# Kernel optimization log

Measured on AMD Instinct MI355X. Metric: run time of the kernel, lower is better.

## Reference

```python
import jax, jax.numpy as jnp
import numpy as np
import math

L, D, H, DH, DFF, V, NB, MAXD = 4, 512, 8, 64, 1024, 32128, 32, 128
B, S = 2, 2048
EPS = 1e-6


def gelu_new(x):
    return 0.5 * x * (1.0 + jnp.tanh(math.sqrt(2.0 / math.pi) * (x + 0.044715 * x ** 3)))


def t5_layernorm(x, w):
    var = jnp.mean(jnp.square(x.astype(jnp.float32)), axis=-1, keepdims=True)
    return w * (x * jax.lax.rsqrt(var + EPS))


def relative_position_bucket(rel_pos, num_buckets=NB, max_distance=MAXD):
    # bidirectional T5 bucketing
    nb = num_buckets // 2
    buckets = (rel_pos > 0).astype(jnp.int32) * nb
    rp = jnp.abs(rel_pos)
    max_exact = nb // 2
    is_small = rp < max_exact
    rp_large = max_exact + (
        jnp.log(jnp.maximum(rp, 1).astype(jnp.float32) / max_exact)
        / math.log(max_distance / max_exact) * (nb - max_exact)
    ).astype(jnp.int32)
    rp_large = jnp.minimum(rp_large, nb - 1)
    return buckets + jnp.where(is_small, rp, rp_large)


def compute_bias(rel_bias_table, q_len, k_len):
    ctx = jnp.arange(q_len)[:, None]
    mem = jnp.arange(k_len)[None, :]
    buckets = relative_position_bucket(mem - ctx)              # [S, S]
    vals = rel_bias_table[buckets]                             # [S, S, H]
    return jnp.transpose(vals, (2, 0, 1))[None]                # [1, H, S, S]


def setup_inputs() -> dict:
    key = jax.random.key(0)
    ks = jax.random.split(key, 12)
    s = 0.02
    return {
        "input_ids": jax.random.randint(ks[0], (B, S), 0, V),
        "embed": jax.random.normal(ks[1], (V, D), jnp.float32) * s,
        "Wq": jax.random.normal(ks[2], (L, D, H * DH), jnp.float32) * s,
        "Wk": jax.random.normal(ks[3], (L, D, H * DH), jnp.float32) * s,
        "Wv": jax.random.normal(ks[4], (L, D, H * DH), jnp.float32) * s,
        "Wo": jax.random.normal(ks[5], (L, H * DH, D), jnp.float32) * s,
        "rel_bias": jax.random.normal(ks[6], (NB, H), jnp.float32) * s,
        "wi0": jax.random.normal(ks[7], (L, D, DFF), jnp.float32) * s,
        "wi1": jax.random.normal(ks[8], (L, D, DFF), jnp.float32) * s,
        "wo_ffn": jax.random.normal(ks[9], (L, DFF, D), jnp.float32) * s,
        "ln0_w": jnp.ones((L, D), jnp.float32),
        "ln1_w": jnp.ones((L, D), jnp.float32),
        "final_ln_w": jnp.ones((D,), jnp.float32),
    }


def encoder_forward(input_ids, embed, Wq, Wk, Wv, Wo, rel_bias, wi0, wi1, wo_ffn, ln0_w, ln1_w, final_ln_w):
    x = embed[input_ids]                                       # [B, S, D]
    pos_bias = compute_bias(rel_bias, S, S)                    # [1, H, S, S], reused across layers
    for i in range(L):
        # --- self-attention (T5: no 1/sqrt(d) scaling) ---
        h = t5_layernorm(x, ln0_w[i])
        q = (h @ Wq[i]).reshape(B, S, H, DH)
        k = (h @ Wk[i]).reshape(B, S, H, DH)
        v = (h @ Wv[i]).reshape(B, S, H, DH)
        scores = jnp.einsum('bqhd,bkhd->bhqk', q, k) + pos_bias
        attn = jax.nn.softmax(scores, axis=-1)
        o = jnp.einsum('bhqk,bkhd->bqhd', attn, v).reshape(B, S, H * DH)
        x = x + o @ Wo[i]
        # --- gated-GELU FFN ---
        h = t5_layernorm(x, ln1_w[i])
        g = gelu_new(h @ wi0[i]) * (h @ wi1[i])
        x = x + g @ wo_ffn[i]
    out = t5_layernorm(x, final_ln_w)
    return out, pos_bias


def reference(input_ids, embed, Wq, Wk, Wv, Wo, rel_bias, wi0, wi1, wo_ffn, ln0_w, ln1_w, final_ln_w):
    return encoder_forward(input_ids, embed, Wq, Wk, Wv, Wo, rel_bias, wi0, wi1, wo_ffn, ln0_w, ln1_w, final_ln_w)
```

## Files before the change

### kernel.cpp

```cpp
#include <hip/hip_runtime.h>

#define NTOK 4096

typedef float f32x4 __attribute__((ext_vector_type(4)));
typedef short s16x8 __attribute__((ext_vector_type(8)));
typedef unsigned short u16x4 __attribute__((ext_vector_type(4)));
typedef unsigned short u16x8 __attribute__((ext_vector_type(8)));

__device__ __forceinline__ unsigned short fbf(float f) {
  unsigned int u = __float_as_uint(f);
  return (unsigned short)((u + 0x7FFFu + ((u >> 16) & 1u)) >> 16);
}
__device__ __forceinline__ float bf2f(unsigned short s) {
  return __uint_as_float(((unsigned int)s) << 16);
}
__device__ __forceinline__ float gelu_new_f(float x) {
  float inner = 0.7978845608028654f * (x + 0.044715f * x * x * x);
  return 0.5f * x * (1.0f + tanhf(inner));
}

__device__ __forceinline__ void gl_lds16(const void* g, void* l) {
  __builtin_amdgcn_global_load_lds(
      (const __attribute__((address_space(1))) unsigned int*)g,
      (__attribute__((address_space(3))) unsigned int*)l, 16, 0, 0);
}

__global__ void embed_kernel(const int* __restrict__ ids, const float* __restrict__ emb,
                             float* __restrict__ x) {
  int tok = blockIdx.x;
  int id = ids[tok];
  int t = threadIdx.x;
  *(float4*)(x + (size_t)tok * 512 + t * 4) = *(const float4*)(emb + (size_t)id * 512 + t * 4);
}

__global__ void build_dbias_kernel(const float* __restrict__ rel_bias, float* __restrict__ dbias) {
  int d = blockIdx.x * 256 + threadIdx.x;
  if (d >= 4096) return;
  int rel = d - 2047;
  int bucket = (rel > 0) ? 16 : 0;
  int rp = rel < 0 ? -rel : rel;
  if (rp < 8) {
    bucket += rp;
  } else {
    float v = logf((float)rp / 8.0f) / logf(16.0f) * 8.0f;
    int rl = 8 + (int)v;
    bucket += (rl < 15) ? rl : 15;
  }
  for (int hh = 0; hh < 8; ++hh)
    dbias[hh * 4096 + d] = rel_bias[bucket * 8 + hh];
}

__global__ void posbias_kernel(const float* __restrict__ dbias, float* __restrict__ out1) {
  size_t g = (size_t)blockIdx.x * 256 + threadIdx.x;
  int k4 = (int)(g & 511) * 4;
  int qq = (int)((g >> 9) & 2047);
  int hh = (int)(g >> 20);
  const float* src = dbias + hh * 4096 + (k4 - qq + 2047);
  *(float4*)(out1 + g * 4) = make_float4(src[0], src[1], src[2], src[3]);
}

__global__ void rmsnorm_bf16_kernel(const float* __restrict__ x, const float* __restrict__ w,
                                    unsigned short* __restrict__ out) {
  int tok = blockIdx.x;
  int t = threadIdx.x;
  float4 v = *(const float4*)(x + (size_t)tok * 512 + t * 4);
  float ss = v.x * v.x + v.y * v.y + v.z * v.z + v.w * v.w;
  for (int m = 1; m < 64; m <<= 1) ss += __shfl_xor(ss, m, 64);
  __shared__ float part[2];
  if ((t & 63) == 0) part[t >> 6] = ss;
  __syncthreads();
  float scale = rsqrtf((part[0] + part[1]) * (1.0f / 512.0f) + 1e-6f);
  float4 wv = *(const float4*)(w + t * 4);
  u16x4 o = {fbf(wv.x * v.x * scale), fbf(wv.y * v.y * scale),
             fbf(wv.z * v.z * scale), fbf(wv.w * v.w * scale)};
  *(u16x4*)(out + (size_t)tok * 512 + t * 4) = o;
}

__global__ void rmsnorm_f32_kernel(const float* __restrict__ x, const float* __restrict__ w,
                                   float* __restrict__ out) {
  int tok = blockIdx.x;
  int t = threadIdx.x;
  float4 v = *(const float4*)(x + (size_t)tok * 512 + t * 4);
  float ss = v.x * v.x + v.y * v.y + v.z * v.z + v.w * v.w;
  for (int m = 1; m < 64; m <<= 1) ss += __shfl_xor(ss, m, 64);
  __shared__ float part[2];
  if ((t & 63) == 0) part[t >> 6] = ss;
  __syncthreads();
  float scale = rsqrtf((part[0] + part[1]) * (1.0f / 512.0f) + 1e-6f);
  float4 wv = *(const float4*)(w + t * 4);
  *(float4*)(out + (size_t)tok * 512 + t * 4) =
      make_float4(wv.x * v.x * scale, wv.y * v.y * scale, wv.z * v.z * scale, wv.w * v.w * scale);
}

__global__ void transw_kernel(const float* S0, const float* S1, const float* S2, const float* S3,
                              unsigned short* D0, unsigned short* D1, unsigned short* D2,
                              unsigned short* D3, int R, int C) {
  __shared__ float tile[32][33];
  int mat = blockIdx.z >> 2, layer = blockIdx.z & 3;
  const float* src = (mat == 0 ? S0 : mat == 1 ? S1 : mat == 2 ? S2 : S3) + (size_t)layer * R * C;
  unsigned short* dst = (mat == 0 ? D0 : mat == 1 ? D1 : mat == 2 ? D2 : D3) + (size_t)layer * R * C;
  int t = threadIdx.x;
  int r0 = blockIdx.y * 32, c0 = blockIdx.x * 32;
  int tr = t >> 3, tc = (t & 7) * 4;
  float4 v = *(const float4*)(src + (size_t)(r0 + tr) * C + c0 + tc);
  tile[tr][tc] = v.x; tile[tr][tc + 1] = v.y; tile[tr][tc + 2] = v.z; tile[tr][tc + 3] = v.w;
  __syncthreads();
  u16x4 o = {fbf(tile[tc + 0][tr]), fbf(tile[tc + 1][tr]),
             fbf(tile[tc + 2][tr]), fbf(tile[tc + 3][tr])};
  *(u16x4*)(dst + (size_t)(c0 + tr) * R + r0 + tc) = o;
}

__global__ __launch_bounds__(256) void gemm64_kernel(
    const unsigned short* __restrict__ A,
    const unsigned short* B0, const unsigned short* B1, const unsigned short* B2,
    void* C0, void* C1, void* C2, const float* __restrict__ Res,
    int M, int N, int K, int m0, int m1, int m2) {
  __shared__ unsigned short As[2][64 * 64];
  __shared__ unsigned short Bs[2][64 * 64];
  const int z = blockIdx.z;
  const unsigned short* B = (z == 0) ? B0 : (z == 1) ? B1 : B2;
  void* Cptr = (z == 0) ? C0 : (z == 1) ? C1 : C2;
  const int mode = (z == 0) ? m0 : (z == 1) ? m1 : m2;
  const int t = threadIdx.x, lane = t & 63, w = t >> 6;
  const int quad = lane >> 4, c = lane & 15;
  const int wr = w >> 1, wc = w & 1;
  const int row0 = blockIdx.y * 64, col0 = blockIdx.x * 64;
  const int ar = t >> 3, aj = t & 7;
  const int asrc8 = (aj ^ (ar & 7)) * 8;
  const unsigned short* Agl = A + (size_t)(row0 + ar) * K + asrc8;
  const unsigned short* Bgl = B + (size_t)(col0 + ar) * K + asrc8;
  f32x4 acc[2][2];
#pragma unroll
  for (int i = 0; i < 2; ++i)
#pragma unroll
    for (int j = 0; j < 2; ++j) { f32x4 zz = {0.f, 0.f, 0.f, 0.f}; acc[i][j] = zz; }

  gl_lds16(Agl, &As[0][w * 512]);
  gl_lds16(Agl + 32 * (size_t)K, &As[0][2048 + w * 512]);
  gl_lds16(Bgl, &Bs[0][w * 512]);
  gl_lds16(Bgl + 32 * (size_t)K, &Bs[0][2048 + w * 512]);
  __syncthreads();

  int p = 0;
  for (int k0 = 0; k0 < K; k0 += 64) {
    if (k0 + 64 < K) {
      gl_lds16(Agl + k0 + 64, &As[p ^ 1][w * 512]);
      gl_lds16(Agl + k0 + 64 + 32 * (size_t)K, &As[p ^ 1][2048 + w * 512]);
      gl_lds16(Bgl + k0 + 64, &Bs[p ^ 1][w * 512]);
      gl_lds16(Bgl + k0 + 64 + 32 * (size_t)K, &Bs[p ^ 1][2048 + w * 512]);
    }
    s16x8 af[2][2], bf[2][2];
#pragma unroll
    for (int rb = 0; rb < 2; ++rb) {
      int r = wr * 32 + rb * 16 + c;
      int n = wc * 32 + rb * 16 + c;
#pragma unroll
      for (int ks = 0; ks < 2; ++ks) {
        af[rb][ks] = *(const s16x8*)&As[p][r * 64 + (((ks * 4 + quad) ^ (r & 7)) << 3)];
        bf[rb][ks] = *(const s16x8*)&Bs[p][n * 64 + (((ks * 4 + quad) ^ (n & 7)) << 3)];
      }
    }
#pragma unroll
    for (int rb = 0; rb < 2; ++rb)
#pragma unroll
      for (int cb = 0; cb < 2; ++cb)
#pragma unroll
        for (int ks = 0; ks < 2; ++ks)
          acc[rb][cb] = __builtin_amdgcn_mfma_f32_16x16x32_bf16(af[rb][ks], bf[cb][ks], acc[rb][cb], 0, 0, 0);
    __syncthreads();
    p ^= 1;
  }

  const int mb = row0 + wr * 32 + quad * 4;
  const int nb = col0 + wc * 32 + c;
  if (mode == 0) {
    unsigned short* Cp = (unsigned short*)Cptr;
#pragma unroll
    for (int rb = 0; rb < 2; ++rb)
#pragma unroll
      for (int cb = 0; cb < 2; ++cb) {
        size_t base = (size_t)(mb + rb * 16) * N + nb + cb * 16;
#pragma unroll
        for (int reg = 0; reg < 4; ++reg) Cp[base + (size_t)reg * N] = fbf(acc[rb][cb][reg]);
      }
  } else if (mode == 1) {
    unsigned short* Cp = (unsigned short*)Cptr;
#pragma unroll
    for (int rb = 0; rb < 2; ++rb)
#pragma unroll
      for (int cb = 0; cb < 2; ++cb) {
        u16x4 pk = {fbf(acc[rb][cb][0]), fbf(acc[rb][cb][1]), fbf(acc[rb][cb][2]), fbf(acc[rb][cb][3])};
        *(u16x4*)&Cp[(size_t)(nb + cb * 16) * M + mb + rb * 16] = pk;
      }
  } else {
    float* Cf = (float*)Cptr;
#pragma unroll
    for (int rb = 0; rb < 2; ++rb)
#pragma unroll
      for (int cb = 0; cb < 2; ++cb)
#pragma unroll
        for (int reg = 0; reg < 4; ++reg) {
          size_t o = (size_t)(mb + rb * 16 + reg) * N + nb + cb * 16;
          Cf[o] = Res[o] + acc[rb][cb][reg];
        }
  }
}

__global__ __launch_bounds__(256) void gemm64_wo_kernel(
    const unsigned short* __restrict__ O0, const unsigned short* __restrict__ O1,
    const float* __restrict__ lsum, const unsigned short* __restrict__ Bw,
    float* __restrict__ Cf, const float* __restrict__ Res) {
  __shared__ unsigned short As[2][64 * 64];
  __shared__ unsigned short Bs[2][64 * 64];
  const int K = 512, N = 512;
  const int t = threadIdx.x, lane = t & 63, w = t >> 6;
  const int quad = lane >> 4, c = lane & 15;
  const int wr = w >> 1, wc = w & 1;
  const int row0 = blockIdx.y * 64, col0 = blockIdx.x * 64;
  const int ar = t >> 3, aj = t & 7;
  const int gc8 = (aj ^ (ar & 7)) * 8;
  const unsigned short* Bgl = Bw + (size_t)(col0 + ar) * K + gc8;

  size_t abase[2];
#pragma unroll
  for (int v = 0; v < 2; ++v) {
    int tok = row0 + ar + 32 * v;
    abase[v] = (size_t)((tok >> 11) * 16384 + (tok & 2047));
  }

  u16x8 ap0[2], ap1[2];
  float asum[2];
  auto ldA = [&](int kt) {
#pragma unroll
    for (int v = 0; v < 2; ++v) {
      size_t gr = abase[v] + (size_t)kt * 2048;
      ap0[v] = *(const u16x8*)(O0 + gr * 64 + gc8);
      ap1[v] = *(const u16x8*)(O1 + gr * 64 + gc8);
      asum[v] = lsum[gr] + lsum[32768 + gr];
    }
  };
  auto wrA = [&](int pp) {
#pragma unroll
    for (int v = 0; v < 2; ++v) {
      float inv = 1.0f / asum[v];
      u16x8 o;
#pragma unroll
      for (int j = 0; j < 8; ++j)
        o[j] = fbf((bf2f(ap0[v][j]) + bf2f(ap1[v][j])) * inv);
      *(u16x8*)&As[pp][(ar + 32 * v) * 64 + aj * 8] = o;
    }
  };

  f32x4 acc[2][2];
#pragma unroll
  for (int i = 0; i < 2; ++i)
#pragma unroll
    for (int j = 0; j < 2; ++j) { f32x4 zz = {0.f, 0.f, 0.f, 0.f}; acc[i][j] = zz; }

  ldA(0);
  wrA(0);
  gl_lds16(Bgl, &Bs[0][w * 512]);
  gl_lds16(Bgl + 32 * (size_t)K, &Bs[0][2048 + w * 512]);
  __syncthreads();
  ldA(1);

  int p = 0;
  for (int i = 0; i < 8; ++i) {
    if (i < 7) {
      int k0n = (i + 1) * 64;
      gl_lds16(Bgl + k0n, &Bs[p ^ 1][w * 512]);
      gl_lds16(Bgl + k0n + 32 * (size_t)K, &Bs[p ^ 1][2048 + w * 512]);
      wrA(p ^ 1);
    }
    s16x8 af[2][2], bf[2][2];
#pragma unroll
    for (int rb = 0; rb < 2; ++rb) {
      int r = wr * 32 + rb * 16 + c;
      int n = wc * 32 + rb * 16 + c;
#pragma unroll
      for (int ks = 0; ks < 2; ++ks) {
        af[rb][ks] = *(const s16x8*)&As[p][r * 64 + (((ks * 4 + quad) ^ (r & 7)) << 3)];
        bf[rb][ks] = *(const s16x8*)&Bs[p][n * 64 + (((ks * 4 + quad) ^ (n & 7)) << 3)];
      }
    }
#pragma unroll
    for (int rb = 0; rb < 2; ++rb)
#pragma unroll
      for (int cb = 0; cb < 2; ++cb)
#pragma unroll
        for (int ks = 0; ks < 2; ++ks)
          acc[rb][cb] = __builtin_amdgcn_mfma_f32_16x16x32_bf16(af[rb][ks], bf[cb][ks], acc[rb][cb], 0, 0, 0);
    if (i < 6) ldA(i + 2);
    __syncthreads();
    p ^= 1;
  }

  const int mb = row0 + wr * 32 + quad * 4;
  const int nb = col0 + wc * 32 + c;
#pragma unroll
  for (int rb = 0; rb < 2; ++rb)
#pragma unroll
    for (int cb = 0; cb < 2; ++cb)
#pragma unroll
      for (int reg = 0; reg < 4; ++reg) {
        size_t o = (size_t)(mb + rb * 16 + reg) * N + nb + cb * 16;
        Cf[o] = Res[o] + acc[rb][cb][reg];
      }
}

__global__ __launch_bounds__(256) void gemm_ffn_kernel(
    const unsigned short* __restrict__ A, const unsigned short* __restrict__ B0g,
    const unsigned short* __restrict__ B1g, unsigned short* __restrict__ C) {
  __shared__ unsigned short As[2][128 * 64];
  __shared__ unsigned short Bs0[2][64 * 64];
  __shared__ unsigned short Bs1[2][64 * 64];
  const int t = threadIdx.x, lane = t & 63, w = t >> 6;
  const int quad = lane >> 4, c = lane & 15;
  const int wr = w >> 1, wc = w & 1;
  const int row0 = blockIdx.y * 128, col0 = blockIdx.x * 64;
  const int K = 512;
  f32x4 acc0[4][2], acc1[4][2];
#pragma unroll
  for (int i = 0; i < 4; ++i)
#pragma unroll
    for (int j = 0; j < 2; ++j) {
      f32x4 zz = {0.f, 0.f, 0.f, 0.f};
      acc0[i][j] = zz; acc1[i][j] = zz;
    }

  const int ar = t >> 3, aj = t & 7;
  const int asrc8 = (aj ^ (ar & 7)) * 8;
  const unsigned short* Agl = A + (size_t)(row0 + ar) * K + asrc8;
  const unsigned short* B0gl = B0g + (size_t)(col0 + ar) * K + asrc8;
  const unsigned short* B1gl = B1g + (size_t)(col0 + ar) * K + asrc8;

  auto stage = [&](int pp, int kk) {
    gl_lds16(Agl + kk, &As[pp][w * 512]);
    gl_lds16(Agl + kk + 32 * (size_t)K, &As[pp][2048 + w * 512]);
    gl_lds16(Agl + kk + 64 * (size_t)K, &As[pp][4096 + w * 512]);
    gl_lds16(Agl + kk + 96 * (size_t)K, &As[pp][6144 + w * 512]);
    gl_lds16(B0gl + kk, &Bs0[pp][w * 512]);
    gl_lds16(B0gl + kk + 32 * (size_t)K, &Bs0[pp][2048 + w * 512]);
    gl_lds16(B1gl + kk, &Bs1[pp][w * 512]);
    gl_lds16(B1gl + kk + 32 * (size_t)K, &Bs1[pp][2048 + w * 512]);
  };

  stage(0, 0);
  __syncthreads();

  int p = 0;
  for (int k0 = 0; k0 < K; k0 += 64) {
    if (k0 + 64 < K) stage(p ^ 1, k0 + 64);
    s16x8 af[4][2], bf0[2][2], bf1[2][2];
#pragma unroll
    for (int rb = 0; rb < 4; ++rb) {
      int r = wr * 64 + rb * 16 + c;
#pragma unroll
      for (int ks = 0; ks < 2; ++ks)
        af[rb][ks] = *(const s16x8*)&As[p][r * 64 + (((ks * 4 + quad) ^ (r & 7)) << 3)];
    }
#pragma unroll
    for (int cb = 0; cb < 2; ++cb) {
      int n = wc * 32 + cb * 16 + c;
#pragma unroll
      for (int ks = 0; ks < 2; ++ks) {
        bf0[cb][ks] = *(const s16x8*)&Bs0[p][n * 64 + (((ks * 4 + quad) ^ (n & 7)) << 3)];
        bf1[cb][ks] = *(const s16x8*)&Bs1[p][n * 64 + (((ks * 4 + quad) ^ (n & 7)) << 3)];
      }
    }
#pragma unroll
    for (int rb = 0; rb < 4; ++rb)
#pragma unroll
      for (int cb = 0; cb < 2; ++cb)
#pragma unroll
        for (int ks = 0; ks < 2; ++ks) {
          acc0[rb][cb] = __builtin_amdgcn_mfma_f32_16x16x32_bf16(af[rb][ks], bf0[cb][ks], acc0[rb][cb], 0, 0, 0);
          acc1[rb][cb] = __builtin_amdgcn_mfma_f32_16x16x32_bf16(af[rb][ks], bf1[cb][ks], acc1[rb][cb], 0, 0, 0);
        }
    __syncthreads();
    p ^= 1;
  }

  const int mb = row0 + wr * 64 + quad * 4;
  const int nb = col0 + wc * 32 + c;
#pragma unroll
  for (int rb = 0; rb < 4; ++rb)
#pragma unroll
    for (int cb = 0; cb < 2; ++cb) {
      size_t base = (size_t)(mb + rb * 16) * 1024 + nb + cb * 16;
#pragma unroll
      for (int reg = 0; reg < 4; ++reg)
        C[base + (size_t)reg * 1024] = fbf(gelu_new_f(acc0[rb][cb][reg]) * acc1[rb][cb][reg]);
    }
}

__global__ __launch_bounds__(256, 4) void attn_split_kernel(
    const unsigned short* __restrict__ qg, const unsigned short* __restrict__ kg,
    const unsigned short* __restrict__ vtg, const float* __restrict__ dbias,
    unsigned short* __restrict__ Op0, unsigned short* __restrict__ Op1,
    float* __restrict__ lsum) {
  __shared__ unsigned short Ks[64 * 64];
  __shared__ unsigned short Vs[64 * 64];
  __shared__ unsigned short Ps[4][16 * 64];
  __shared__ float Bb[128];
  const int b = blockIdx.z, hh = blockIdx.y;
  const int q0b = (blockIdx.x & 31) * 64;
  const int split = blockIdx.x >> 5;
  unsigned short* Op = (split == 0) ? Op0 : Op1;
  const int t = threadIdx.x, lane = t & 63, w = t >> 6;
  const int quad = lane >> 4, c = lane & 15;
  const int hd = hh * 64;
  s16x8 qf[2];
#pragma unroll
  for (int ks = 0; ks < 2; ++ks)
    qf[ks] = *(const s16x8*)(qg + (size_t)(b * 2048 + q0b + w * 16 + c) * 512 + hd + ks * 32 + quad * 8);
  f32x4 oacc[4];
  float psum[4];
#pragma unroll
  for (int i = 0; i < 4; ++i) {
    f32x4 zz = {0.f, 0.f, 0.f, 0.f};
    oacc[i] = zz; psum[i] = 0.f;
  }
  const int biasbase = hh * 4096 + 2047 - q0b - 63;
  const int rowloc = w * 16 + quad * 4;
  const int srow = t >> 3, sjj = t & 7;
  const unsigned short* kbase = kg + (size_t)(b * 2048) * 512 + hd;
  const unsigned short* vbase = vtg + (size_t)hd * 4096 + b * 2048;
  const int kt0 = split * 16;

  s16x8 kpre[2], vpre[2];
  float bpre;
  {
    int k0 = kt0 * 64;
#pragma unroll
    for (int v = 0; v < 2; ++v) {
      int row = srow + 32 * v;
      kpre[v] = *(const s16x8*)(kbase + (size_t)(k0 + row) * 512 + sjj * 8);
      vpre[v] = *(const s16x8*)(vbase + (size_t)row * 4096 + k0 + sjj * 8);
    }
    bpre = dbias[biasbase + k0 + (t & 127)];
  }

  for (int kt = kt0; kt < kt0 + 16; ++kt) {
    __syncthreads();
#pragma unroll
    for (int v = 0; v < 2; ++v) {
      int row = srow + 32 * v;
      int ch = (sjj ^ (row & 7)) << 3;
      *(s16x8*)&Ks[row * 64 + ch] = kpre[v];
      *(s16x8*)&Vs[row * 64 + ch] = vpre[v];
    }
    if (t < 128) Bb[t] = bpre;
    __syncthreads();
    {
      int k0n = (kt + 1 < kt0 + 16) ? (kt + 1) * 64 : kt * 64;
#pragma unroll
      for (int v = 0; v < 2; ++v) {
        int row = srow + 32 * v;
        kpre[v] = *(const s16x8*)(kbase + (size_t)(k0n + row) * 512 + sjj * 8);
        vpre[v] = *(const s16x8*)(vbase + (size_t)row * 4096 + k0n + sjj * 8);
      }
      bpre = dbias[biasbase + k0n + (t & 127)];
    }

    f32x4 s[4];
#pragma unroll
    for (int i = 0; i < 4; ++i) { f32x4 zz = {0.f, 0.f, 0.f, 0.f}; s[i] = zz; }
#pragma unroll
    for (int ks = 0; ks < 2; ++ks)
#pragma unroll
      for (int cb = 0; cb < 4; ++cb) {
        int n = cb * 16 + c;
        s16x8 kf = *(const s16x8*)&Ks[n * 64 + (((ks * 4 + quad) ^ (n & 7)) << 3)];
        s[cb] = __builtin_amdgcn_mfma_f32_16x16x32_bf16(qf[ks], kf, s[cb], 0, 0, 0);
      }
#pragma unroll
    for (int cb = 0; cb < 4; ++cb) {
      int col = cb * 16 + c;
      int chunkbase = (col >> 3);
#pragma unroll
      for (int reg = 0; reg < 4; ++reg) {
        float pp = __expf(s[cb][reg] + Bb[col - rowloc - reg + 63]);
        psum[reg] += pp;
        int rowp = quad * 4 + reg;
        Ps[w][rowp * 64 + ((chunkbase ^ (rowp & 7)) << 3) + (col & 7)] = fbf(pp);
      }
    }
#pragma unroll
    for (int ks = 0; ks < 2; ++ks) {
      s16x8 pf = *(const s16x8*)&Ps[w][c * 64 + (((ks * 4 + quad) ^ (c & 7)) << 3)];
#pragma unroll
      for (int cbo = 0; cbo < 4; ++cbo) {
        int n = cbo * 16 + c;
        s16x8 vf = *(const s16x8*)&Vs[n * 64 + (((ks * 4 + quad) ^ (n & 7)) << 3)];
        oacc[cbo] = __builtin_amdgcn_mfma_f32_16x16x32_bf16(pf, vf, oacc[cbo], 0, 0, 0);
      }
    }
  }
#pragma unroll
  for (int reg = 0; reg < 4; ++reg) {
    float ps = psum[reg];
    ps += __shfl_xor(ps, 1, 64);
    ps += __shfl_xor(ps, 2, 64);
    ps += __shfl_xor(ps, 4, 64);
    ps += __shfl_xor(ps, 8, 64);
    psum[reg] = ps;
  }
  const size_t obase = ((size_t)(b * 8 + hh) * 2048 + q0b + w * 16 + quad * 4);
#pragma unroll
  for (int cbo = 0; cbo < 4; ++cbo)
#pragma unroll
    for (int reg = 0; reg < 4; ++reg)
      Op[(obase + reg) * 64 + cbo * 16 + c] = fbf(oacc[cbo][reg]);
  if (c == 0) {
    const size_t lbase = (size_t)split * 32768 + (size_t)(b * 8 + hh) * 2048 + q0b + w * 16 + quad * 4;
#pragma unroll
    for (int reg = 0; reg < 4; ++reg) lsum[lbase + reg] = psum[reg];
  }
}

extern "C" void kernel_launch(void* const* d_in, const int* in_sizes, int n_in,
                              void* d_out, int out_size, void* d_ws, size_t ws_size,
                              hipStream_t stream) {
  const int*   ids      = (const int*)d_in[0];
  const float* embed    = (const float*)d_in[1];
  const float* Wq       = (const float*)d_in[2];
  const float* Wk       = (const float*)d_in[3];
  const float* Wv       = (const float*)d_in[4];
  const float* Wo       = (const float*)d_in[5];
  const float* rel_bias = (const float*)d_in[6];
  const float* wi0      = (const float*)d_in[7];
  const float* wi1      = (const float*)d_in[8];
  const float* wo_ffn   = (const float*)d_in[9];
  const float* ln0      = (const float*)d_in[10];
  const float* ln1      = (const float*)d_in[11];
  const float* final_ln = (const float*)d_in[12];
  float* out = (float*)d_out;
  char* wsb = (char*)d_ws;

  float*          x    = (float*)wsb;
  unsigned short* h    = (unsigned short*)(wsb + 8388608);
  unsigned short* qb   = (unsigned short*)(wsb + 12582912);
  unsigned short* kb   = (unsigned short*)(wsb + 16777216);
  unsigned short* vt   = (unsigned short*)(wsb + 20971520);
  unsigned short* wqT  = (unsigned short*)(wsb + 33554432);
  unsigned short* wkT  = (unsigned short*)(wsb + 35651584);
  unsigned short* wvT  = (unsigned short*)(wsb + 37748736);
  unsigned short* woT  = (unsigned short*)(wsb + 39845888);
  unsigned short* wi0T = (unsigned short*)(wsb + 41943040);
  unsigned short* wi1T = (unsigned short*)(wsb + 46137344);
  unsigned short* wofT = (unsigned short*)(wsb + 50331648);
  float*          dbias= (float*)(wsb + 54525952);
  unsigned short* t0b  = kb;
  unsigned short* Op0  = h;
  unsigned short* Op1  = (unsigned short*)(wsb + 25165824);
  float*          lsum = (float*)(wsb + 60817408);

  embed_kernel<<<NTOK, 128, 0, stream>>>(ids, embed, x);
  build_dbias_kernel<<<16, 256, 0, stream>>>(rel_bias, dbias);
  posbias_kernel<<<32768, 256, 0, stream>>>(dbias, out + 2097152);
  transw_kernel<<<dim3(16, 16, 16), 256, 0, stream>>>(Wq, Wk, Wv, Wo, wqT, wkT, wvT, woT, 512, 512);
  transw_kernel<<<dim3(32, 16, 8), 256, 0, stream>>>(wi0, wi1, wi0, wi0, wi0T, wi1T, wi0T, wi0T, 512, 1024);
  transw_kernel<<<dim3(16, 32, 4), 256, 0, stream>>>(wo_ffn, wo_ffn, wo_ffn, wo_ffn, wofT, wofT, wofT, wofT, 1024, 512);

  for (int l = 0; l < 4; ++l) {
    const unsigned short* wqT_l = wqT + (size_t)l * 262144;
    const unsigned short* wkT_l = wkT + (size_t)l * 262144;
    const unsigned short* wvT_l = wvT + (size_t)l * 262144;
    const unsigned short* woT_l = woT + (size_t)l * 262144;
    const unsigned short* wi0T_l = wi0T + (size_t)l * 524288;
    const unsigned short* wi1T_l = wi1T + (size_t)l * 524288;
    const unsigned short* wofT_l = wofT + (size_t)l * 524288;

    rmsnorm_bf16_kernel<<<NTOK, 128, 0, stream>>>(x, ln0 + l * 512, h);
    gemm64_kernel<<<dim3(8, 64, 3), 256, 0, stream>>>(h, wqT_l, wkT_l, wvT_l,
        qb, kb, vt, nullptr, NTOK, 512, 512, 0, 0, 1);
    attn_split_kernel<<<dim3(64, 8, 2), 256, 0, stream>>>(qb, kb, vt, dbias,
        Op0, Op1, lsum);
    gemm64_wo_kernel<<<dim3(8, 64), 256, 0, stream>>>(Op0, Op1, lsum, woT_l, x, x);
    rmsnorm_bf16_kernel<<<NTOK, 128, 0, stream>>>(x, ln1 + l * 512, h);
    gemm_ffn_kernel<<<dim3(16, 32), 256, 0, stream>>>(h, wi0T_l, wi1T_l, t0b);
    gemm64_kernel<<<dim3(8, 64, 1), 256, 0, stream>>>(t0b, wofT_l, wofT_l, wofT_l,
        x, x, x, x, NTOK, 512, 1024, 2, 2, 2);
  }
  rmsnorm_f32_kernel<<<NTOK, 128, 0, stream>>>(x, final_ln, out);
}
```

Baseline: 674.0 us.

## Fuse RMSNorm into GEMM prologues with sum-of-squares computed in residual epilogues

```diff
diff --git a/kernel.cpp b/kernel.cpp
--- a/kernel.cpp
+++ b/kernel.cpp
@@ -25,12 +25,23 @@
       (__attribute__((address_space(3))) unsigned int*)l, 16, 0, 0);
 }
 
+__global__ void zero_ssq_kernel(float* __restrict__ p) {
+  p[blockIdx.x * 256 + threadIdx.x] = 0.f;
+}
+
 __global__ void embed_kernel(const int* __restrict__ ids, const float* __restrict__ emb,
-                             float* __restrict__ x) {
+                             float* __restrict__ x, float* __restrict__ ssq0) {
   int tok = blockIdx.x;
   int id = ids[tok];
   int t = threadIdx.x;
-  *(float4*)(x + (size_t)tok * 512 + t * 4) = *(const float4*)(emb + (size_t)id * 512 + t * 4);
+  float4 v = *(const float4*)(emb + (size_t)id * 512 + t * 4);
+  *(float4*)(x + (size_t)tok * 512 + t * 4) = v;
+  float ss = v.x * v.x + v.y * v.y + v.z * v.z + v.w * v.w;
+  for (int m = 1; m < 64; m <<= 1) ss += __shfl_xor(ss, m, 64);
+  __shared__ float part[2];
+  if ((t & 63) == 0) part[t >> 6] = ss;
+  __syncthreads();
+  if (t == 0) ssq0[tok] = part[0] + part[1];
 }
 
 __global__ void build_dbias_kernel(const float* __restrict__ rel_bias, float* __restrict__ dbias) {
@@ -59,34 +70,12 @@
   *(float4*)(out1 + g * 4) = make_float4(src[0], src[1], src[2], src[3]);
 }
 
-__global__ void rmsnorm_bf16_kernel(const float* __restrict__ x, const float* __restrict__ w,
-                                    unsigned short* __restrict__ out) {
+__global__ void rmsnorm_f32_kernel(const float* __restrict__ x, const float* __restrict__ w,
+                                   const float* __restrict__ ssqv, float* __restrict__ out) {
   int tok = blockIdx.x;
   int t = threadIdx.x;
+  float scale = rsqrtf(ssqv[tok] * (1.0f / 512.0f) + 1e-6f);
   float4 v = *(const float4*)(x + (size_t)tok * 512 + t * 4);
-  float ss = v.x * v.x + v.y * v.y + v.z * v.z + v.w * v.w;
-  for (int m = 1; m < 64; m <<= 1) ss += __shfl_xor(ss, m, 64);
-  __shared__ float part[2];
-  if ((t & 63) == 0) part[t >> 6] = ss;
-  __syncthreads();
-  float scale = rsqrtf((part[0] + part[1]) * (1.0f / 512.0f) + 1e-6f);
-  float4 wv = *(const float4*)(w + t * 4);
-  u16x4 o = {fbf(wv.x * v.x * scale), fbf(wv.y * v.y * scale),
-             fbf(wv.z * v.z * scale), fbf(wv.w * v.w * scale)};
-  *(u16x4*)(out + (size_t)tok * 512 + t * 4) = o;
-}
-
-__global__ void rmsnorm_f32_kernel(const float* __restrict__ x, const float* __restrict__ w,
-                                   float* __restrict__ out) {
-  int tok = blockIdx.x;
-  int t = threadIdx.x;
-  float4 v = *(const float4*)(x + (size_t)tok * 512 + t * 4);
-  float ss = v.x * v.x + v.y * v.y + v.z * v.z + v.w * v.w;
-  for (int m = 1; m < 64; m <<= 1) ss += __shfl_xor(ss, m, 64);
-  __shared__ float part[2];
-  if ((t & 63) == 0) part[t >> 6] = ss;
-  __syncthreads();
-  float scale = rsqrtf((part[0] + part[1]) * (1.0f / 512.0f) + 1e-6f);
   float4 wv = *(const float4*)(w + t * 4);
   *(float4*)(out + (size_t)tok * 512 + t * 4) =
       make_float4(wv.x * v.x * scale, wv.y * v.y * scale, wv.z * v.z * scale, wv.w * v.w * scale);
@@ -110,44 +99,69 @@
   *(u16x4*)(dst + (size_t)(c0 + tr) * R + r0 + tc) = o;
 }
 
-__global__ __launch_bounds__(256) void gemm64_kernel(
-    const unsigned short* __restrict__ A,
+__global__ __launch_bounds__(256) void gemm64_qkv_kernel(
+    const float* __restrict__ X, const float* __restrict__ lnw, const float* __restrict__ ssqv,
     const unsigned short* B0, const unsigned short* B1, const unsigned short* B2,
-    void* C0, void* C1, void* C2, const float* __restrict__ Res,
-    int M, int N, int K, int m0, int m1, int m2) {
+    unsigned short* __restrict__ Cq, unsigned short* __restrict__ Ck,
+    unsigned short* __restrict__ Cv) {
   __shared__ unsigned short As[2][64 * 64];
   __shared__ unsigned short Bs[2][64 * 64];
+  const int K = 512, N = 512, M = NTOK;
   const int z = blockIdx.z;
   const unsigned short* B = (z == 0) ? B0 : (z == 1) ? B1 : B2;
-  void* Cptr = (z == 0) ? C0 : (z == 1) ? C1 : C2;
-  const int mode = (z == 0) ? m0 : (z == 1) ? m1 : m2;
   const int t = threadIdx.x, lane = t & 63, w = t >> 6;
   const int quad = lane >> 4, c = lane & 15;
   const int wr = w >> 1, wc = w & 1;
   const int row0 = blockIdx.y * 64, col0 = blockIdx.x * 64;
   const int ar = t >> 3, aj = t & 7;
-  const int asrc8 = (aj ^ (ar & 7)) * 8;
-  const unsigned short* Agl = A + (size_t)(row0 + ar) * K + asrc8;
-  const unsigned short* Bgl = B + (size_t)(col0 + ar) * K + asrc8;
+  const int chunk = aj ^ (ar & 7);
+  const unsigned short* Bgl = B + (size_t)(col0 + ar) * K + chunk * 8;
+
+  float scl[2];
+#pragma unroll
+  for (int v = 0; v < 2; ++v)
+    scl[v] = rsqrtf(ssqv[row0 + ar + 32 * v] * (1.0f / 512.0f) + 1e-6f);
+
+  float4 xv[2][2], wv_[2];
+  auto ldA = [&](int kt) {
+    const float* xp = X + (size_t)(row0 + ar) * 512 + kt * 64 + chunk * 8;
+    xv[0][0] = *(const float4*)xp; xv[0][1] = *(const float4*)(xp + 4);
+    xp += 32 * 512;
+    xv[1][0] = *(const float4*)xp; xv[1][1] = *(const float4*)(xp + 4);
+    const float* wp = lnw + kt * 64 + chunk * 8;
+    wv_[0] = *(const float4*)wp; wv_[1] = *(const float4*)(wp + 4);
+  };
+  auto wrA = [&](int pp) {
+#pragma unroll
+    for (int v = 0; v < 2; ++v) {
+      u16x8 o;
+      o[0] = fbf(xv[v][0].x * scl[v] * wv_[0].x); o[1] = fbf(xv[v][0].y * scl[v] * wv_[0].y);
+      o[2] = fbf(xv[v][0].z * scl[v] * wv_[0].z); o[3] = fbf(xv[v][0].w * scl[v] * wv_[0].w);
+      o[4] = fbf(xv[v][1].x * scl[v] * wv_[1].x); o[5] = fbf(xv[v][1].y * scl[v] * wv_[1].y);
+      o[6] = fbf(xv[v][1].z * scl[v] * wv_[1].z); o[7] = fbf(xv[v][1].w * scl[v] * wv_[1].w);
+      *(u16x8*)&As[pp][(ar + 32 * v) * 64 + aj * 8] = o;
+    }
+  };
+
   f32x4 acc[2][2];
 #pragma unroll
   for (int i = 0; i < 2; ++i)
 #pragma unroll
     for (int j = 0; j < 2; ++j) { f32x4 zz = {0.f, 0.f, 0.f, 0.f}; acc[i][j] = zz; }
 
-  gl_lds16(Agl, &As[0][w * 512]);
-  gl_lds16(Agl + 32 * (size_t)K, &As[0][2048 + w * 512]);
+  ldA(0);
+  wrA(0);
   gl_lds16(Bgl, &Bs[0][w * 512]);
   gl_lds16(Bgl + 32 * (size_t)K, &Bs[0][2048 + w * 512]);
   __syncthreads();
+  ldA(1);
 
   int p = 0;
-  for (int k0 = 0; k0 < K; k0 += 64) {
-    if (k0 + 64 < K) {
-      gl_lds16(Agl + k0 + 64, &As[p ^ 1][w * 512]);
-      gl_lds16(Agl + k0 + 64 + 32 * (size_t)K, &As[p ^ 1][2048 + w * 512]);
-      gl_lds16(Bgl + k0 + 64, &Bs[p ^ 1][w * 512]);
-      gl_lds16(Bgl + k0 + 64 + 32 * (size_t)K, &Bs[p ^ 1][2048 + w * 512]);
+  for (int i = 0; i < 8; ++i) {
+    if (i < 7) {
+      gl_lds16(Bgl + (i + 1) * 64, &Bs[p ^ 1][w * 512]);
+      gl_lds16(Bgl + (i + 1) * 64 + 32 * (size_t)K, &Bs[p ^ 1][2048 + w * 512]);
+      wrA(p ^ 1);
     }
     s16x8 af[2][2], bf[2][2];
 #pragma unroll
@@ -167,14 +181,15 @@
 #pragma unroll
         for (int ks = 0; ks < 2; ++ks)
           acc[rb][cb] = __builtin_amdgcn_mfma_f32_16x16x32_bf16(af[rb][ks], bf[cb][ks], acc[rb][cb], 0, 0, 0);
+    if (i < 6) ldA(i + 2);
     __syncthreads();
     p ^= 1;
   }
 
   const int mb = row0 + wr * 32 + quad * 4;
   const int nb = col0 + wc * 32 + c;
-  if (mode == 0) {
-    unsigned short* Cp = (unsigned short*)Cptr;
+  if (z <= 1) {
+    unsigned short* Cp = (z == 0) ? Cq : Ck;
 #pragma unroll
     for (int rb = 0; rb < 2; ++rb)
 #pragma unroll
@@ -183,33 +198,21 @@
 #pragma unroll
         for (int reg = 0; reg < 4; ++reg) Cp[base + (size_t)reg * N] = fbf(acc[rb][cb][reg]);
       }
-  } else if (mode == 1) {
-    unsigned short* Cp = (unsigned short*)Cptr;
+  } else {
 #pragma unroll
     for (int rb = 0; rb < 2; ++rb)
 #pragma unroll
       for (int cb = 0; cb < 2; ++cb) {
         u16x4 pk = {fbf(acc[rb][cb][0]), fbf(acc[rb][cb][1]), fbf(acc[rb][cb][2]), fbf(acc[rb][cb][3])};
-        *(u16x4*)&Cp[(size_t)(nb + cb * 16) * M + mb + rb * 16] = pk;
-      }
-  } else {
-    float* Cf = (float*)Cptr;
-#pragma unroll
-    for (int rb = 0; rb < 2; ++rb)
-#pragma unroll
-      for (int cb = 0; cb < 2; ++cb)
-#pragma unroll
-        for (int reg = 0; reg < 4; ++reg) {
-          size_t o = (size_t)(mb + rb * 16 + reg) * N + nb + cb * 16;
-          Cf[o] = Res[o] + acc[rb][cb][reg];
-        }
+        *(u16x4*)&Cv[(size_t)(nb + cb * 16) * M + mb + rb * 16] = pk;
+      }
   }
 }
 
 __global__ __launch_bounds__(256) void gemm64_wo_kernel(
     const unsigned short* __restrict__ O0, const unsigned short* __restrict__ O1,
     const float* __restrict__ lsum, const unsigned short* __restrict__ Bw,
-    float* __restrict__ Cf, const float* __restrict__ Res) {
+    float* __restrict__ Cf, const float* __restrict__ Res, float* __restrict__ ssqo) {
   __shared__ unsigned short As[2][64 * 64];
   __shared__ unsigned short Bs[2][64 * 64];
   const int K = 512, N = 512;
@@ -300,57 +303,95 @@
 #pragma unroll
   for (int rb = 0; rb < 2; ++rb)
 #pragma unroll
-    for (int cb = 0; cb < 2; ++cb)
-#pragma unroll
-      for (int reg = 0; reg < 4; ++reg) {
+    for (int reg = 0; reg < 4; ++reg) {
+      float vv[2];
+#pragma unroll
+      for (int cb = 0; cb < 2; ++cb) {
         size_t o = (size_t)(mb + rb * 16 + reg) * N + nb + cb * 16;
-        Cf[o] = Res[o] + acc[rb][cb][reg];
-      }
+        float v = Res[o] + acc[rb][cb][reg];
+        Cf[o] = v;
+        vv[cb] = v;
+      }
+      float s = vv[0] * vv[0] + vv[1] * vv[1];
+      s += __shfl_xor(s, 1, 64);
+      s += __shfl_xor(s, 2, 64);
+      s += __shfl_xor(s, 4, 64);
+      s += __shfl_xor(s, 8, 64);
+      if (c == 0) atomicAdd(&ssqo[mb + rb * 16 + reg], s);
+    }
 }
 
 __global__ __launch_bounds__(256) void gemm_ffn_kernel(
-    const unsigned short* __restrict__ A, const unsigned short* __restrict__ B0g,
-    const unsigned short* __restrict__ B1g, unsigned short* __restrict__ C) {
+    const float* __restrict__ X, const float* __restrict__ lnw, const float* __restrict__ ssqv,
+    const unsigned short* __restrict__ B0g, const unsigned short* __restrict__ B1g,
+    unsigned short* __restrict__ C) {
   __shared__ unsigned short As[2][128 * 64];
   __shared__ unsigned short Bs0[2][64 * 64];
   __shared__ unsigned short Bs1[2][64 * 64];
+  const int K = 512;
   const int t = threadIdx.x, lane = t & 63, w = t >> 6;
   const int quad = lane >> 4, c = lane & 15;
   const int wr = w >> 1, wc = w & 1;
   const int row0 = blockIdx.y * 128, col0 = blockIdx.x * 64;
-  const int K = 512;
-  f32x4 acc0[4][2], acc1[4][2];
-#pragma unroll
-  for (int i = 0; i < 4; ++i)
-#pragma unroll
-    for (int j = 0; j < 2; ++j) {
-      f32x4 zz = {0.f, 0.f, 0.f, 0.f};
-      acc0[i][j] = zz; acc1[i][j] = zz;
-    }
-
   const int ar = t >> 3, aj = t & 7;
-  const int asrc8 = (aj ^ (ar & 7)) * 8;
-  const unsigned short* Agl = A + (size_t)(row0 + ar) * K + asrc8;
-  const unsigned short* B0gl = B0g + (size_t)(col0 + ar) * K + asrc8;
-  const unsigned short* B1gl = B1g + (size_t)(col0 + ar) * K + asrc8;
-
-  auto stage = [&](int pp, int kk) {
-    gl_lds16(Agl + kk, &As[pp][w * 512]);
-    gl_lds16(Agl + kk + 32 * (size_t)K, &As[pp][2048 + w * 512]);
-    gl_lds16(Agl + kk + 64 * (size_t)K, &As[pp][4096 + w * 512]);
-    gl_lds16(Agl + kk + 96 * (size_t)K, &As[pp][6144 + w * 512]);
+  const int chunk = aj ^ (ar & 7);
+  const unsigned short* B0gl = B0g + (size_t)(col0 + ar) * K + chunk * 8;
+  const unsigned short* B1gl = B1g + (size_t)(col0 + ar) * K + chunk * 8;
+
+  float scl[4];
+#pragma unroll
+  for (int v = 0; v < 4; ++v)
+    scl[v] = rsqrtf(ssqv[row0 + ar + 32 * v] * (1.0f / 512.0f) + 1e-6f);
+
+  float4 xv[4][2], wv_[2];
+  auto ldA = [&](int kt) {
+#pragma unroll
+    for (int v = 0; v < 4; ++v) {
+      const float* xp = X + (size_t)(row0 + ar + 32 * v) * 512 + kt * 64 + chunk * 8;
+      xv[v][0] = *(const float4*)xp; xv[v][1] = *(const float4*)(xp + 4);
+    }
+    const float* wp = lnw + kt * 64 + chunk * 8;
+    wv_[0] = *(const float4*)wp; wv_[1] = *(const float4*)(wp + 4);
+  };
+  auto wrA = [&](int pp) {
+#pragma unroll
+    for (int v = 0; v < 4; ++v) {
+      u16x8 o;
+      o[0] = fbf(xv[v][0].x * scl[v] * wv_[0].x); o[1] = fbf(xv[v][0].y * scl[v] * wv_[0].y);
+      o[2] = fbf(xv[v][0].z * scl[v] * wv_[0].z); o[3] = fbf(xv[v][0].w * scl[v] * wv_[0].w);
+      o[4] = fbf(xv[v][1].x * scl[v] * wv_[1].x); o[5] = fbf(xv[v][1].y * scl[v] * wv_[1].y);
+      o[6] = fbf(xv[v][1].z * scl[v] * wv_[1].z); o[7] = fbf(xv[v][1].w * scl[v] * wv_[1].w);
+      *(u16x8*)&As[pp][(ar + 32 * v) * 64 + aj * 8] = o;
+    }
+  };
+  auto stageB = [&](int pp, int kk) {
     gl_lds16(B0gl + kk, &Bs0[pp][w * 512]);
     gl_lds16(B0gl + kk + 32 * (size_t)K, &Bs0[pp][2048 + w * 512]);
     gl_lds16(B1gl + kk, &Bs1[pp][w * 512]);
     gl_lds16(B1gl + kk + 32 * (size_t)K, &Bs1[pp][2048 + w * 512]);
   };
 
-  stage(0, 0);
+  f32x4 acc0[4][2], acc1[4][2];
+#pragma unroll
+  for (int i = 0; i < 4; ++i)
+#pragma unroll
+    for (int j = 0; j < 2; ++j) {
+      f32x4 zz = {0.f, 0.f, 0.f, 0.f};
+      acc0[i][j] = zz; acc1[i][j] = zz;
+    }
+
+  ldA(0);
+  wrA(0);
+  stageB(0, 0);
   __syncthreads();
+  ldA(1);
 
   int p = 0;
-  for (int k0 = 0; k0 < K; k0 += 64) {
-    if (k0 + 64 < K) stage(p ^ 1, k0 + 64);
+  for (int i = 0; i < 8; ++i) {
+    if (i < 7) {
+      stageB(p ^ 1, (i + 1) * 64);
+      wrA(p ^ 1);
+    }
     s16x8 af[4][2], bf0[2][2], bf1[2][2];
 #pragma unroll
     for (int rb = 0; rb < 4; ++rb) {
@@ -377,6 +418,7 @@
           acc0[rb][cb] = __builtin_amdgcn_mfma_f32_16x16x32_bf16(af[rb][ks], bf0[cb][ks], acc0[rb][cb], 0, 0, 0);
           acc1[rb][cb] = __builtin_amdgcn_mfma_f32_16x16x32_bf16(af[rb][ks], bf1[cb][ks], acc1[rb][cb], 0, 0, 0);
         }
+    if (i < 6) ldA(i + 2);
     __syncthreads();
     p ^= 1;
   }
@@ -394,7 +436,86 @@
     }
 }
 
-__global__ __launch_bounds__(256, 4) void attn_split_kernel(
+__global__ __launch_bounds__(256) void gemm64_res_kernel(
+    const unsigned short* __restrict__ A, const unsigned short* __restrict__ Bw,
+    float* __restrict__ Cf, const float* __restrict__ Res, float* __restrict__ ssqo, int K) {
+  __shared__ unsigned short As[2][64 * 64];
+  __shared__ unsigned short Bs[2][64 * 64];
+  const int N = 512;
+  const int t = threadIdx.x, lane = t & 63, w = t >> 6;
+  const int quad = lane >> 4, c = lane & 15;
+  const int wr = w >> 1, wc = w & 1;
+  const int row0 = blockIdx.y * 64, col0 = blockIdx.x * 64;
+  const int ar = t >> 3, aj = t & 7;
+  const int asrc8 = (aj ^ (ar & 7)) * 8;
+  const unsigned short* Agl = A + (size_t)(row0 + ar) * K + asrc8;
+  const unsigned short* Bgl = Bw + (size_t)(col0 + ar) * K + asrc8;
+  f32x4 acc[2][2];
+#pragma unroll
+  for (int i = 0; i < 2; ++i)
+#pragma unroll
+    for (int j = 0; j < 2; ++j) { f32x4 zz = {0.f, 0.f, 0.f, 0.f}; acc[i][j] = zz; }
+
+  gl_lds16(Agl, &As[0][w * 512]);
+  gl_lds16(Agl + 32 * (size_t)K, &As[0][2048 + w * 512]);
+  gl_lds16(Bgl, &Bs[0][w * 512]);
+  gl_lds16(Bgl + 32 * (size_t)K, &Bs[0][2048 + w * 512]);
+  __syncthreads();
+
+  int p = 0;
+  for (int k0 = 0; k0 < K; k0 += 64) {
+    if (k0 + 64 < K) {
+      gl_lds16(Agl + k0 + 64, &As[p ^ 1][w * 512]);
+      gl_lds16(Agl + k0 + 64 + 32 * (size_t)K, &As[p ^ 1][2048 + w * 512]);
+      gl_lds16(Bgl + k0 + 64, &Bs[p ^ 1][w * 512]);
+      gl_lds16(Bgl + k0 + 64 + 32 * (size_t)K, &Bs[p ^ 1][2048 + w * 512]);
+    }
+    s16x8 af[2][2], bf[2][2];
+#pragma unroll
+    for (int rb = 0; rb < 2; ++rb) {
+      int r = wr * 32 + rb * 16 + c;
+      int n = wc * 32 + rb * 16 + c;
+#pragma unroll
+      for (int ks = 0; ks < 2; ++ks) {
+        af[rb][ks] = *(const s16x8*)&As[p][r * 64 + (((ks * 4 + quad) ^ (r & 7)) << 3)];
+        bf[rb][ks] = *(const s16x8*)&Bs[p][n * 64 + (((ks * 4 + quad) ^ (n & 7)) << 3)];
+      }
+    }
+#pragma unroll
+    for (int rb = 0; rb < 2; ++rb)
+#pragma unroll
+      for (int cb = 0; cb < 2; ++cb)
+#pragma unroll
+        for (int ks = 0; ks < 2; ++ks)
+          acc[rb][cb] = __builtin_amdgcn_mfma_f32_16x16x32_bf16(af[rb][ks], bf[cb][ks], acc[rb][cb], 0, 0, 0);
+    __syncthreads();
+    p ^= 1;
+  }
+
+  const int mb = row0 + wr * 32 + quad * 4;
+  const int nb = col0 + wc * 32 + c;
+#pragma unroll
+  for (int rb = 0; rb < 2; ++rb)
+#pragma unroll
+    for (int reg = 0; reg < 4; ++reg) {
+      float vv[2];
+#pragma unroll
+      for (int cb = 0; cb < 2; ++cb) {
+        size_t o = (size_t)(mb + rb * 16 + reg) * N + nb + cb * 16;
+        float v = Res[o] + acc[rb][cb][reg];
+        Cf[o] = v;
+        vv[cb] = v;
+      }
+      float s = vv[0] * vv[0] + vv[1] * vv[1];
+      s += __shfl_xor(s, 1, 64);
+      s += __shfl_xor(s, 2, 64);
+      s += __shfl_xor(s, 4, 64);
+      s += __shfl_xor(s, 8, 64);
+      if (c == 0) atomicAdd(&ssqo[mb + rb * 16 + reg], s);
+    }
+}
+
+__global__ __launch_bounds__(256) void attn_split_kernel(
     const unsigned short* __restrict__ qg, const unsigned short* __restrict__ kg,
     const unsigned short* __restrict__ vtg, const float* __restrict__ dbias,
     unsigned short* __restrict__ Op0, unsigned short* __restrict__ Op1,
@@ -555,8 +676,10 @@
   unsigned short* Op0  = h;
   unsigned short* Op1  = (unsigned short*)(wsb + 25165824);
   float*          lsum = (float*)(wsb + 60817408);
-
-  embed_kernel<<<NTOK, 128, 0, stream>>>(ids, embed, x);
+  float*          ssq  = (float*)(wsb + 61079552);
+
+  zero_ssq_kernel<<<144, 256, 0, stream>>>(ssq);
+  embed_kernel<<<NTOK, 128, 0, stream>>>(ids, embed, x, ssq);
   build_dbias_kernel<<<16, 256, 0, stream>>>(rel_bias, dbias);
   posbias_kernel<<<32768, 256, 0, stream>>>(dbias, out + 2097152);
   transw_kernel<<<dim3(16, 16, 16), 256, 0, stream>>>(Wq, Wk, Wv, Wo, wqT, wkT, wvT, woT, 512, 512);
@@ -571,17 +694,18 @@
     const unsigned short* wi0T_l = wi0T + (size_t)l * 524288;
     const unsigned short* wi1T_l = wi1T + (size_t)l * 524288;
     const unsigned short* wofT_l = wofT + (size_t)l * 524288;
-
-    rmsnorm_bf16_kernel<<<NTOK, 128, 0, stream>>>(x, ln0 + l * 512, h);
-    gemm64_kernel<<<dim3(8, 64, 3), 256, 0, stream>>>(h, wqT_l, wkT_l, wvT_l,
-        qb, kb, vt, nullptr, NTOK, 512, 512, 0, 0, 1);
+    const float* ssq_in = ssq + (size_t)(2 * l) * 4096;
+    float* ssq_wo = ssq + (size_t)(2 * l + 1) * 4096;
+    float* ssq_fo = ssq + (size_t)(2 * l + 2) * 4096;
+
+    gemm64_qkv_kernel<<<dim3(8, 64, 3), 256, 0, stream>>>(x, ln0 + l * 512, ssq_in,
+        wqT_l, wkT_l, wvT_l, qb, kb, vt);
     attn_split_kernel<<<dim3(64, 8, 2), 256, 0, stream>>>(qb, kb, vt, dbias,
         Op0, Op1, lsum);
-    gemm64_wo_kernel<<<dim3(8, 64), 256, 0, stream>>>(Op0, Op1, lsum, woT_l, x, x);
-    rmsnorm_bf16_kernel<<<NTOK, 128, 0, stream>>>(x, ln1 + l * 512, h);
-    gemm_ffn_kernel<<<dim3(16, 32), 256, 0, stream>>>(h, wi0T_l, wi1T_l, t0b);
-    gemm64_kernel<<<dim3(8, 64, 1), 256, 0, stream>>>(t0b, wofT_l, wofT_l, wofT_l,
-        x, x, x, x, NTOK, 512, 1024, 2, 2, 2);
-  }
-  rmsnorm_f32_kernel<<<NTOK, 128, 0, stream>>>(x, final_ln, out);
-}
+    gemm64_wo_kernel<<<dim3(8, 64), 256, 0, stream>>>(Op0, Op1, lsum, woT_l, x, x, ssq_wo);
+    gemm_ffn_kernel<<<dim3(16, 32), 256, 0, stream>>>(x, ln1 + l * 512, ssq_wo,
+        wi0T_l, wi1T_l, t0b);
+    gemm64_res_kernel<<<dim3(8, 64), 256, 0, stream>>>(t0b, wofT_l, x, x, ssq_fo, 1024);
+  }
+  rmsnorm_f32_kernel<<<NTOK, 128, 0, stream>>>(x, final_ln, ssq + 8 * 4096, out);
+}
```

New measurement: 736.6 us. +9.3%, slower.
